# Performance work log

Measured on AMD Instinct MI355X. Metric: run time of the kernel, lower is better.

The kernel has to match this reference:

```python
import jax, jax.numpy as jnp
import numpy as np

N = 100000      # nodes
E = 1600000     # edges (avg degree 16)
IN, HID, OUT = 128, 32, 16
H = 2           # attention heads
EPS = 1e-5
NEG_SLOPE = 0.2


def setup_inputs() -> dict:
    key = jax.random.key(0)
    ks = jax.random.split(key, 24)
    f32 = jnp.float32
    def w(k, shape, scale=0.1):
        return jax.random.normal(k, shape, f32) * scale
    return {
        "x": jax.random.normal(ks[0], (N, IN), f32),
        "edge_index": jax.random.randint(ks[1], (2, E), 0, N, dtype=jnp.int32),
        # GCN layer 1
        "gcn1_W": w(ks[2], (IN, HID)), "gcn1_b": w(ks[3], (HID,)),
        # BN1 (eval mode: running stats)
        "bn1_g": 1.0 + w(ks[4], (HID,)), "bn1_b": w(ks[5], (HID,)),
        "bn1_m": w(ks[6], (HID,)), "bn1_v": 1.0 + jnp.abs(w(ks[7], (HID,))),
        # GAT layer 1 (HID -> HID, heads=H, concat=False)
        "gat1_W": w(ks[8], (HID, H * HID)), "gat1_as": w(ks[9], (H, HID)),
        "gat1_ad": w(ks[10], (H, HID)), "gat1_b": w(ks[11], (HID,)),
        # GCN layer 2
        "gcn2_W": w(ks[12], (HID, HID)), "gcn2_b": w(ks[13], (HID,)),
        # BN2
        "bn2_g": 1.0 + w(ks[14], (HID,)), "bn2_b": w(ks[15], (HID,)),
        "bn2_m": w(ks[16], (HID,)), "bn2_v": 1.0 + jnp.abs(w(ks[17], (HID,))),
        # GAT layer 2 (HID -> OUT, heads=H, concat=False)
        "gat2_W": w(ks[18], (HID, H * OUT)), "gat2_as": w(ks[19], (H, OUT)),
        "gat2_ad": w(ks[20], (H, OUT)), "gat2_b": w(ks[21], (OUT,)),
    }


def _add_self_loops(edge_index):
    loop = jnp.arange(N, dtype=edge_index.dtype)
    src = jnp.concatenate([edge_index[0], loop])
    dst = jnp.concatenate([edge_index[1], loop])
    return src, dst


def _gcn(x, src, dst, W, b):
    h = x @ W                                             # [N, F]
    deg = jax.ops.segment_sum(jnp.ones_like(dst, h.dtype), dst, N)
    dinv = jax.lax.rsqrt(jnp.maximum(deg, 1.0))
    norm = dinv[src] * dinv[dst]                          # [Etot]
    out = jax.ops.segment_sum(h[src] * norm[:, None], dst, N)
    return out + b


def _gat(x, src, dst, W, a_src, a_dst, b, F):
    # PyG GATConv (concat=False -> mean over heads); eval mode (no attn dropout)
    h = (x @ W).reshape(N, H, F)                          # [N, H, F]
    al_s = jnp.einsum('nhf,hf->nh', h, a_src)             # [N, H]
    al_d = jnp.einsum('nhf,hf->nh', h, a_dst)
    e = jax.nn.leaky_relu(al_s[src] + al_d[dst], NEG_SLOPE)  # [Etot, H]
    # segment softmax over destination neighborhoods (self-loops ensure >=1 edge)
    m = jax.ops.segment_max(e, dst, N)
    ex = jnp.exp(e - m[dst])
    s = jax.ops.segment_sum(ex, dst, N)
    alpha = ex / s[dst]                                   # [Etot, H]
    out = jax.ops.segment_sum(alpha[:, :, None] * h[src], dst, N)  # [N, H, F]
    return out.mean(axis=1) + b


def _bn_eval(x, g, b, m, v):
    return (x - m) * jax.lax.rsqrt(v + EPS) * g + b


def reference(x, edge_index, gcn1_W, gcn1_b, bn1_g, bn1_b, bn1_m, bn1_v,
              gat1_W, gat1_as, gat1_ad, gat1_b, gcn2_W, gcn2_b,
              bn2_g, bn2_b, bn2_m, bn2_v, gat2_W, gat2_as, gat2_ad, gat2_b):
    src, dst = _add_self_loops(edge_index)
    h = _gcn(x, src, dst, gcn1_W, gcn1_b)
    h = jax.nn.relu(_bn_eval(h, bn1_g, bn1_b, bn1_m, bn1_v))
    h = jax.nn.relu(_gat(h, src, dst, gat1_W, gat1_as, gat1_ad, gat1_b, HID))
    h = _gcn(h, src, dst, gcn2_W, gcn2_b)
    h = jax.nn.relu(_bn_eval(h, bn2_g, bn2_b, bn2_m, bn2_v))
    h = _gat(h, src, dst, gat2_W, gat2_as, gat2_ad, gat2_b, OUT)
    return jax.nn.log_softmax(h, axis=1)
```

## Files before the change

### kernel.cpp

```cpp
#include <hip/hip_runtime.h>
#include <hip/hip_bf16.h>

#define NN 100000
#define EE 1600000
#define SLAB 64
#define KB 391
#define CHUNK 4096

static constexpr float EPSV = 1e-5f;
static constexpr float SLOPE = 0.2f;

__device__ __forceinline__ float lrelu(float v) { return v > 0.f ? v : SLOPE * v; }

__device__ __forceinline__ unsigned rne_bf16(float v) {
    unsigned u = __float_as_uint(v);
    return (u + 0x7fffu + ((u >> 16) & 1u)) >> 16;
}
__device__ __forceinline__ float bf16_lo(unsigned u) { return __uint_as_float(u << 16); }
__device__ __forceinline__ float bf16_hi(unsigned u) { return __uint_as_float(u & 0xffff0000u); }


__global__ void k_z(int* __restrict__ hist) {
    int i = threadIdx.x;
    if (i < KB) hist[i] = 0;
}

__global__ __launch_bounds__(256) void k_hist(const int* __restrict__ dst, int* __restrict__ hist) {
    __shared__ int h[KB];
    int tid = threadIdx.x;
    for (int i = tid; i < KB; i += 256) h[i] = 0;
    __syncthreads();
    int e0 = blockIdx.x * CHUNK;
    #pragma unroll
    for (int r = 0; r < CHUNK / 256; ++r) {
        int e = e0 + r * 256 + tid;
        if (e < EE) atomicAdd(&h[dst[e] >> 8], 1);
    }
    __syncthreads();
    for (int i = tid; i < KB; i += 256)
        if (h[i]) atomicAdd(&hist[i], h[i]);
}

__global__ __launch_bounds__(512) void k_scan(const int* __restrict__ hist,
                                              int* __restrict__ start, int* __restrict__ gcur) {
    __shared__ int h[KB];
    int tid = threadIdx.x;
    for (int i = tid; i < KB; i += 512) h[i] = hist[i];
    __syncthreads();
    for (int t = tid; t < KB; t += 512) {
        int s = 0;
        for (int i = 0; i < t; ++i) s += h[i];
        start[t] = s;
        gcur[t] = 0;
    }
}

__global__ __launch_bounds__(256) void k_scat(const int* __restrict__ src, const int* __restrict__ dst,
                                              const int* __restrict__ start, int* __restrict__ gcur,
                                              unsigned int* __restrict__ ebuf) {
    __shared__ int hc[KB], hb[KB];
    int tid = threadIdx.x;
    for (int i = tid; i < KB; i += 256) hc[i] = 0;
    __syncthreads();
    int e0 = blockIdx.x * CHUNK;
    #pragma unroll
    for (int r = 0; r < CHUNK / 256; ++r) {
        int e = e0 + r * 256 + tid;
        if (e < EE) atomicAdd(&hc[dst[e] >> 8], 1);
    }
    __syncthreads();
    for (int i = tid; i < KB; i += 256) {
        int c = hc[i];
        if (c) hb[i] = atomicAdd(&gcur[i], c);
        hc[i] = 0;
    }
    __syncthreads();
    #pragma unroll
    for (int r = 0; r < CHUNK / 256; ++r) {
        int e = e0 + r * 256 + tid;
        if (e < EE) {
            int d = dst[e];
            int b = d >> 8;
            int rk = atomicAdd(&hc[b], 1);
            ebuf[start[b] + hb[b] + rk] = ((unsigned)src[e] << 8) | (unsigned)(d & 255);
        }
    }
}

__global__ __launch_bounds__(256) void k_bucket(const unsigned int* __restrict__ ebuf,
                                                const int* __restrict__ start, const int* __restrict__ hist,
                                                int* __restrict__ col, int* __restrict__ cnt) {
    __shared__ int lc[256];
    int tid = threadIdx.x;
    int b = blockIdx.x;
    lc[tid] = 0;
    __syncthreads();
    int s = start[b], nb = hist[b];
    for (int i = tid; i < nb; i += 256) {
        unsigned v = ebuf[s + i];
        int l = v & 255;
        int r = atomicAdd(&lc[l], 1);
        col[(((b << 8) + l) << 6) + r] = v >> 8;
    }
    __syncthreads();
    int node = (b << 8) + tid;
    if (node < NN) cnt[node] = lc[tid];
}

__global__ void k_deg(const int* __restrict__ cnt, float* __restrict__ dinv,
                      int* __restrict__ col) {
    int i = blockIdx.x * 256 + threadIdx.x;
    if (i < NN) {
        int c = cnt[i];
        dinv[i] = rsqrtf((float)(c + 1));
        col[i * SLAB + c] = i;
    }
}


__global__ __launch_bounds__(256) void k_gemm1(const float* __restrict__ x,
                                               const float* __restrict__ W,
                                               const float* __restrict__ dinv,
                                               unsigned* __restrict__ hsp) {
    __shared__ float xs[64][128];
    int tid = threadIdx.x;
    int lane = tid & 63;
    int wv = tid >> 6;
    int khalf = lane >> 5, f = lane & 31;
    float wreg[64];
    const float* wp = W + (khalf * 64) * 32 + f;
    #pragma unroll
    for (int i = 0; i < 64; ++i) wreg[i] = wp[i * 32];
    int n0 = blockIdx.x * 64;
    for (int i = tid; i < 64 * 32; i += 256) {
        int row = i >> 5, c4 = i & 31;
        int n = n0 + row;
        float4 v = (n < NN) ? *(const float4*)&x[(size_t)n * 128 + c4 * 4]
                            : make_float4(0.f, 0.f, 0.f, 0.f);
        *(float4*)&xs[row][c4 * 4] = v;
    }
    __syncthreads();
    #pragma unroll 4
    for (int t = 0; t < 16; ++t) {
        int row = wv * 16 + t;
        int n = n0 + row;
        if (n >= NN) break;
        const float* xp = &xs[row][khalf * 64];
        float a0 = 0.f, a1 = 0.f, a2 = 0.f, a3 = 0.f;
        #pragma unroll
        for (int j = 0; j < 16; j += 4) {
            float4 v0 = *(const float4*)&xp[(j + 0) * 4];
            float4 v1 = *(const float4*)&xp[(j + 1) * 4];
            float4 v2 = *(const float4*)&xp[(j + 2) * 4];
            float4 v3 = *(const float4*)&xp[(j + 3) * 4];
            a0 += v0.x * wreg[j * 4 + 0]  + v0.y * wreg[j * 4 + 1]  + v0.z * wreg[j * 4 + 2]  + v0.w * wreg[j * 4 + 3];
            a1 += v1.x * wreg[j * 4 + 4]  + v1.y * wreg[j * 4 + 5]  + v1.z * wreg[j * 4 + 6]  + v1.w * wreg[j * 4 + 7];
            a2 += v2.x * wreg[j * 4 + 8]  + v2.y * wreg[j * 4 + 9]  + v2.z * wreg[j * 4 + 10] + v2.w * wreg[j * 4 + 11];
            a3 += v3.x * wreg[j * 4 + 12] + v3.y * wreg[j * 4 + 13] + v3.z * wreg[j * 4 + 14] + v3.w * wreg[j * 4 + 15];
        }
        float tot = (a0 + a1) + (a2 + a3);
        tot += __shfl_xor(tot, 32);
        unsigned r16 = rne_bf16(tot * dinv[n]);
        unsigned hi16 = __shfl(r16, f + 1, 32);
        if (khalf == 0 && !(f & 1))
            hsp[n * 16 + (f >> 1)] = (hi16 << 16) | (r16 & 0xffffu);
    }
}


__global__ __launch_bounds__(256) void k_gcn1_gat1t(
    const unsigned* __restrict__ hsp, const int* __restrict__ cnt,
    const int* __restrict__ col, const float* __restrict__ dinv,
    const float* __restrict__ gb, const float* __restrict__ bng,
    const float* __restrict__ bnb, const float* __restrict__ bnm,
    const float* __restrict__ bnv,
    const float* __restrict__ W1, const float* __restrict__ as_, const float* __restrict__ ad_,
    unsigned* __restrict__ gp, float* __restrict__ al) {
    __shared__ float wAs[32][32], wBs[32][32];
    int tid = threadIdx.x;
    for (int i = tid; i < 1024; i += 256) {
        int k = i >> 5, f = i & 31;
        wAs[k][f] = W1[k * 64 + f];
        wBs[k][f] = W1[k * 64 + 32 + f];
    }
    __syncthreads();
    int r = tid >> 5, lane = tid & 31;
    int half = lane >> 4, l16 = lane & 15;
    int n = blockIdx.x * 8 + r;
    int dn = cnt[n] + 1;
    int base = n * SLAB;
    int c0 = col[base + lane];
    int c1 = (dn > 32) ? col[base + 32 + lane] : 0;
    float aL0 = 0.f, aH0 = 0.f, aL1 = 0.f, aH1 = 0.f;
    for (int j2 = 0; j2 < dn; j2 += 4) {
        int eA = j2 + half, eB = j2 + 2 + half;
        int cA = __shfl((j2 < 32) ? c0 : c1, eA & 31, 32);
        int cB = __shfl((j2 + 2 < 32) ? c0 : c1, eB & 31, 32);
        bool okA = eA < dn, okB = eB < dn;
        cA = okA ? cA : 0; cB = okB ? cB : 0;
        unsigned uA = hsp[cA * 16 + l16];
        unsigned uB = hsp[cB * 16 + l16];
        uA = okA ? uA : 0u; uB = okB ? uB : 0u;
        aL0 += bf16_lo(uA); aH0 += bf16_hi(uA);
        aL1 += bf16_lo(uB); aH1 += bf16_hi(uB);
    }
    float accLo = aL0 + aL1, accHi = aH0 + aH1;
    accLo += __shfl_xor(accLo, 16);
    accHi += __shfl_xor(accHi, 16);
    float vLo = __shfl(accLo, lane >> 1, 32);
    float vHi = __shfl(accHi, lane >> 1, 32);
    float acc = (lane & 1) ? vHi : vLo;
    float v = dinv[n] * acc + gb[lane];
    v = (v - bnm[lane]) * rsqrtf(bnv[lane] + EPSV) * bng[lane] + bnb[lane];
    v = fmaxf(v, 0.f);
    float gA0 = 0.f, gA1 = 0.f, gB0 = 0.f, gB1 = 0.f;
    #pragma unroll
    for (int k = 0; k < 32; k += 2) {
        float t0 = __shfl(v, k, 32);
        float t1v = __shfl(v, k + 1, 32);
        gA0 += t0 * wAs[k][lane];     gB0 += t0 * wBs[k][lane];
        gA1 += t1v * wAs[k + 1][lane]; gB1 += t1v * wBs[k + 1][lane];
    }
    float gA = gA0 + gA1, gB = gB0 + gB1;
    float pas0 = gA * as_[lane],      pad0 = gA * ad_[lane];
    float pas1 = gB * as_[32 + lane], pad1 = gB * ad_[32 + lane];
    #pragma unroll
    for (int off = 16; off; off >>= 1) {
        pas0 += __shfl_xor(pas0, off);
        pad0 += __shfl_xor(pad0, off);
        pas1 += __shfl_xor(pas1, off);
        pad1 += __shfl_xor(pad1, off);
    }
    if (lane == 0) *(float4*)&al[n * 4] = make_float4(pas0, pas1, pad0, pad1);
    gp[n * 32 + lane] = (rne_bf16(gB) << 16) | rne_bf16(gA);
}


__global__ __launch_bounds__(256) void k_gat1_pv(
    const unsigned* __restrict__ gp, const float* __restrict__ al,
    const int* __restrict__ cnt, const int* __restrict__ col,
    const float* __restrict__ b, const float* __restrict__ W2,
    const float* __restrict__ dinv, unsigned* __restrict__ hs3p) {
    __shared__ float2 ec[8][SLAB];
    __shared__ float w2s[32][32];
    int tid = threadIdx.x;
    for (int i = tid; i < 1024; i += 256) w2s[i >> 5][i & 31] = W2[i];
    __syncthreads();
    int r = tid >> 5, lane = tid & 31;
    int half = lane >> 4, l16 = lane & 15;
    int n = blockIdx.x * 8 + r;
    int dn = cnt[n] + 1;
    int base = n * SLAB;
    int c0 = col[base + lane];
    int c1 = (dn > 32) ? col[base + 32 + lane] : 0;
    float ad0 = al[n * 4 + 2], ad1 = al[n * 4 + 3];
    float e0a = -1e30f, e1a = -1e30f, e0b = -1e30f, e1b = -1e30f;
    if (lane < dn) {
        float4 a4 = *(const float4*)&al[(size_t)c0 * 4];
        e0a = lrelu(a4.x + ad0); e1a = lrelu(a4.y + ad1);
    }
    if (32 + lane < dn) {
        float4 a4 = *(const float4*)&al[(size_t)c1 * 4];
        e0b = lrelu(a4.x + ad0); e1b = lrelu(a4.y + ad1);
    }
    float m0 = fmaxf(e0a, e0b), m1 = fmaxf(e1a, e1b);
    #pragma unroll
    for (int off = 16; off; off >>= 1) {
        m0 = fmaxf(m0, __shfl_xor(m0, off));
        m1 = fmaxf(m1, __shfl_xor(m1, off));
    }
    float x0a = (lane < dn) ? __expf(e0a - m0) : 0.f;
    float x1a = (lane < dn) ? __expf(e1a - m1) : 0.f;
    float x0b = (32 + lane < dn) ? __expf(e0b - m0) : 0.f;
    float x1b = (32 + lane < dn) ? __expf(e1b - m1) : 0.f;
    ec[r][lane] = make_float2(x0a, x1a);
    ec[r][32 + lane] = make_float2(x0b, x1b);
    float s0 = x0a + x0b, s1 = x1a + x1b;
    #pragma unroll
    for (int off = 16; off; off >>= 1) {
        s0 += __shfl_xor(s0, off);
        s1 += __shfl_xor(s1, off);
    }
    const uint2* gp2 = (const uint2*)gp;
    float a0L = 0.f, a0H = 0.f, a1L = 0.f, a1H = 0.f;
    float b0L = 0.f, b0H = 0.f, b1L = 0.f, b1H = 0.f;
    for (int j2 = 0; j2 < dn; j2 += 4) {
        int eA = j2 + half, eB = j2 + 2 + half;
        int cA = __shfl((j2 < 32) ? c0 : c1, eA & 31, 32);
        int cB = __shfl((j2 + 2 < 32) ? c0 : c1, eB & 31, 32);
        bool okA = eA < dn, okB = eB < dn;
        cA = okA ? cA : 0; cB = okB ? cB : 0;
        uint2 uA = gp2[cA * 16 + l16];
        uint2 uB = gp2[cB * 16 + l16];
        float2 wA = ec[r][eA & 63];
        float2 wB = ec[r][eB & 63];
        uA.x = okA ? uA.x : 0u; uA.y = okA ? uA.y : 0u;
        uB.x = okB ? uB.x : 0u; uB.y = okB ? uB.y : 0u;
        a0L += wA.x * bf16_lo(uA.x); a1L += wA.y * bf16_hi(uA.x);
        a0H += wA.x * bf16_lo(uA.y); a1H += wA.y * bf16_hi(uA.y);
        b0L += wB.x * bf16_lo(uB.x); b1L += wB.y * bf16_hi(uB.x);
        b0H += wB.x * bf16_lo(uB.y); b1H += wB.y * bf16_hi(uB.y);
    }
    a0L += b0L; a0H += b0H; a1L += b1L; a1H += b1H;
    a0L += __shfl_xor(a0L, 16); a0H += __shfl_xor(a0H, 16);
    a1L += __shfl_xor(a1L, 16); a1H += __shfl_xor(a1H, 16);
    int p = lane >> 1;
    float t0L = __shfl(a0L, p, 32), t0H = __shfl(a0H, p, 32);
    float t1L = __shfl(a1L, p, 32), t1H = __shfl(a1H, p, 32);
    float A0 = (lane & 1) ? t0H : t0L;
    float A1 = (lane & 1) ? t1H : t1L;
    float v = 0.5f * (A0 / s0 + A1 / s1) + b[lane];
    v = fmaxf(v, 0.f);
    float g0 = 0.f, g1 = 0.f;
    #pragma unroll
    for (int k = 0; k < 32; k += 2) {
        g0 += __shfl(v, k, 32) * w2s[k][lane];
        g1 += __shfl(v, k + 1, 32) * w2s[k + 1][lane];
    }
    unsigned r16 = rne_bf16((g0 + g1) * dinv[n]);
    unsigned hi16 = __shfl(r16, lane + 1, 32);
    if (!(lane & 1)) hs3p[n * 16 + (lane >> 1)] = (hi16 << 16) | (r16 & 0xffffu);
}


__global__ __launch_bounds__(256) void k_gcn2_gat2t(
    const unsigned* __restrict__ hsp, const int* __restrict__ cnt,
    const int* __restrict__ col, const float* __restrict__ dinv,
    const float* __restrict__ gb, const float* __restrict__ bng,
    const float* __restrict__ bnb, const float* __restrict__ bnm,
    const float* __restrict__ bnv,
    const float* __restrict__ Wg, const float* __restrict__ as_, const float* __restrict__ ad_,
    unsigned* __restrict__ g2p, float* __restrict__ al) {
    __shared__ float wgs[32][32];
    int tid = threadIdx.x;
    for (int i = tid; i < 1024; i += 256) wgs[i >> 5][i & 31] = Wg[i];
    __syncthreads();
    int r = tid >> 5, lane = tid & 31;
    int half = lane >> 4, l16 = lane & 15;
    int n = blockIdx.x * 8 + r;
    int dn = cnt[n] + 1;
    int base = n * SLAB;
    int c0 = col[base + lane];
    int c1 = (dn > 32) ? col[base + 32 + lane] : 0;
    float aL0 = 0.f, aH0 = 0.f, aL1 = 0.f, aH1 = 0.f;
    for (int j2 = 0; j2 < dn; j2 += 4) {
        int eA = j2 + half, eB = j2 + 2 + half;
        int cA = __shfl((j2 < 32) ? c0 : c1, eA & 31, 32);
        int cB = __shfl((j2 + 2 < 32) ? c0 : c1, eB & 31, 32);
        bool okA = eA < dn, okB = eB < dn;
        cA = okA ? cA : 0; cB = okB ? cB : 0;
        unsigned uA = hsp[cA * 16 + l16];
        unsigned uB = hsp[cB * 16 + l16];
        uA = okA ? uA : 0u; uB = okB ? uB : 0u;
        aL0 += bf16_lo(uA); aH0 += bf16_hi(uA);
        aL1 += bf16_lo(uB); aH1 += bf16_hi(uB);
    }
    float accLo = aL0 + aL1, accHi = aH0 + aH1;
    accLo += __shfl_xor(accLo, 16);
    accHi += __shfl_xor(accHi, 16);
    float vLo = __shfl(accLo, lane >> 1, 32);
    float vHi = __shfl(accHi, lane >> 1, 32);
    float acc = (lane & 1) ? vHi : vLo;
    float v = dinv[n] * acc + gb[lane];
    v = (v - bnm[lane]) * rsqrtf(bnv[lane] + EPSV) * bng[lane] + bnb[lane];
    v = fmaxf(v, 0.f);
    float g0 = 0.f, g1 = 0.f;
    #pragma unroll
    for (int k = 0; k < 32; k += 2) {
        g0 += __shfl(v, k, 32) * wgs[k][lane];
        g1 += __shfl(v, k + 1, 32) * wgs[k + 1][lane];
    }
    float g = g0 + g1;
    int hh = lane >> 4, ff = lane & 15;
    float as_v = g * as_[hh * 16 + ff];
    float ad_v = g * ad_[hh * 16 + ff];
    #pragma unroll
    for (int off = 8; off; off >>= 1) {
        as_v += __shfl_xor(as_v, off);
        ad_v += __shfl_xor(ad_v, off);
    }
    if (ff == 0) { al[n * 4 + hh] = as_v; al[n * 4 + 2 + hh] = ad_v; }
    unsigned r16 = rne_bf16(g);
    unsigned hi16 = __shfl(r16, lane + 1, 32);
    if (!(lane & 1)) g2p[n * 16 + (lane >> 1)] = (hi16 << 16) | (r16 & 0xffffu);
}


__global__ __launch_bounds__(256) void k_gat2_agg(
    const unsigned* __restrict__ g2p, const float* __restrict__ al,
    const int* __restrict__ cnt, const int* __restrict__ col,
    const float* __restrict__ b, float* __restrict__ out) {
    __shared__ float2 ec[8][SLAB];
    int tid = threadIdx.x;
    int r = tid >> 5, lane = tid & 31;
    int half = lane >> 4, l16 = lane & 15;
    int n = blockIdx.x * 8 + r;
    int dn = cnt[n] + 1;
    int base = n * SLAB;
    int c0 = col[base + lane];
    int c1 = (dn > 32) ? col[base + 32 + lane] : 0;
    float ad0 = al[n * 4 + 2], ad1 = al[n * 4 + 3];
    float e0a = -1e30f, e1a = -1e30f, e0b = -1e30f, e1b = -1e30f;
    if (lane < dn) {
        float4 a4 = *(const float4*)&al[(size_t)c0 * 4];
        e0a = lrelu(a4.x + ad0); e1a = lrelu(a4.y + ad1);
    }
    if (32 + lane < dn) {
        float4 a4 = *(const float4*)&al[(size_t)c1 * 4];
        e0b = lrelu(a4.x + ad0); e1b = lrelu(a4.y + ad1);
    }
    float m0 = fmaxf(e0a, e0b), m1 = fmaxf(e1a, e1b);
    #pragma unroll
    for (int off = 16; off; off >>= 1) {
        m0 = fmaxf(m0, __shfl_xor(m0, off));
        m1 = fmaxf(m1, __shfl_xor(m1, off));
    }
    float x0a = (lane < dn) ? __expf(e0a - m0) : 0.f;
    float x1a = (lane < dn) ? __expf(e1a - m1) : 0.f;
    float x0b = (32 + lane < dn) ? __expf(e0b - m0) : 0.f;
    float x1b = (32 + lane < dn) ? __expf(e1b - m1) : 0.f;
    ec[r][lane] = make_float2(x0a, x1a);
    ec[r][32 + lane] = make_float2(x0b, x1b);
    float s0 = x0a + x0b, s1 = x1a + x1b;
    #pragma unroll
    for (int off = 16; off; off >>= 1) {
        s0 += __shfl_xor(s0, off);
        s1 += __shfl_xor(s1, off);
    }
    bool head1 = (l16 & 8) != 0;
    float aL0 = 0.f, aH0 = 0.f, aL1 = 0.f, aH1 = 0.f;
    for (int j2 = 0; j2 < dn; j2 += 4) {
        int eA = j2 + half, eB = j2 + 2 + half;
        int cA = __shfl((j2 < 32) ? c0 : c1, eA & 31, 32);
        int cB = __shfl((j2 + 2 < 32) ? c0 : c1, eB & 31, 32);
        bool okA = eA < dn, okB = eB < dn;
        cA = okA ? cA : 0; cB = okB ? cB : 0;
        unsigned uA = g2p[cA * 16 + l16];
        unsigned uB = g2p[cB * 16 + l16];
        float2 wA = ec[r][eA & 63];
        float2 wB = ec[r][eB & 63];
        float wa = head1 ? wA.y : wA.x;
        float wb = head1 ? wB.y : wB.x;
        uA = okA ? uA : 0u; uB = okB ? uB : 0u;
        aL0 += wa * bf16_lo(uA); aH0 += wa * bf16_hi(uA);
        aL1 += wb * bf16_lo(uB); aH1 += wb * bf16_hi(uB);
    }
    float accLo = aL0 + aL1, accHi = aH0 + aH1;
    accLo += __shfl_xor(accLo, 16);
    accHi += __shfl_xor(accHi, 16);
    float vLo = __shfl(accLo, lane >> 1, 32);
    float vHi = __shfl(accHi, lane >> 1, 32);
    float acc = (lane & 1) ? vHi : vLo;
    int hh = lane >> 4, ff = lane & 15;
    acc /= (hh ? s1 : s0);
    float v = 0.5f * (acc + __shfl_xor(acc, 16)) + b[ff];
    float mx = v;
    #pragma unroll
    for (int off = 8; off; off >>= 1) mx = fmaxf(mx, __shfl_xor(mx, off));
    float se = __expf(v - mx);
    #pragma unroll
    for (int off = 8; off; off >>= 1) se += __shfl_xor(se, off);
    if (hh == 0) out[(size_t)n * 16 + ff] = v - mx - __logf(se);
}


static inline size_t al256(size_t x) { return (x + 255) & ~((size_t)255); }

extern "C" void kernel_launch(void* const* d_in, const int* in_sizes, int n_in,
                              void* d_out, int out_size, void* d_ws, size_t ws_size,
                              hipStream_t stream) {
    const float* x      = (const float*)d_in[0];
    const int*   ei     = (const int*)d_in[1];
    const float* gcn1_W = (const float*)d_in[2];
    const float* gcn1_b = (const float*)d_in[3];
    const float* bn1_g  = (const float*)d_in[4];
    const float* bn1_b  = (const float*)d_in[5];
    const float* bn1_m  = (const float*)d_in[6];
    const float* bn1_v  = (const float*)d_in[7];
    const float* gat1_W = (const float*)d_in[8];
    const float* gat1_as= (const float*)d_in[9];
    const float* gat1_ad= (const float*)d_in[10];
    const float* gat1_b = (const float*)d_in[11];
    const float* gcn2_W = (const float*)d_in[12];
    const float* gcn2_b = (const float*)d_in[13];
    const float* bn2_g  = (const float*)d_in[14];
    const float* bn2_b  = (const float*)d_in[15];
    const float* bn2_m  = (const float*)d_in[16];
    const float* bn2_v  = (const float*)d_in[17];
    const float* gat2_W = (const float*)d_in[18];
    const float* gat2_as= (const float*)d_in[19];
    const float* gat2_ad= (const float*)d_in[20];
    const float* gat2_b = (const float*)d_in[21];
    float* out = (float*)d_out;

    char* w = (char*)d_ws;
    size_t off = 0;
    auto alloc = [&](size_t bytes) { void* p = w + off; off = al256(off + bytes); return p; };
    int*      cnt   = (int*)alloc((size_t)NN * 4);
    float*    dinv  = (float*)alloc((size_t)NN * 4);
    int*      col   = (int*)alloc((size_t)NN * SLAB * 4);
    unsigned* hsp   = (unsigned*)alloc((size_t)NN * 16 * 4);
    unsigned* g1p   = (unsigned*)alloc((size_t)NN * 32 * 4);
    unsigned* g2p   = (unsigned*)alloc((size_t)NN * 16 * 4);
    float*    al    = (float*)alloc((size_t)NN * 4 * 4);
    int*      hist  = (int*)alloc((size_t)KB * 4);
    int*      start = (int*)alloc((size_t)KB * 4);
    int*      gcur  = (int*)alloc((size_t)KB * 4);
    unsigned int* ebuf = (unsigned int*)g1p;

    const int* esrc = ei;
    const int* edst = ei + EE;
    const int GE = (EE + CHUNK - 1) / CHUNK;

    k_z<<<1, 512, 0, stream>>>(hist);
    k_hist<<<GE, 256, 0, stream>>>(edst, hist);
    k_scan<<<1, 512, 0, stream>>>(hist, start, gcur);
    k_scat<<<GE, 256, 0, stream>>>(esrc, edst, start, gcur, ebuf);
    k_bucket<<<KB, 256, 0, stream>>>(ebuf, start, hist, col, cnt);
    k_deg<<<(NN + 255) / 256, 256, 0, stream>>>(cnt, dinv, col);

    k_gemm1<<<(NN + 63) / 64, 256, 0, stream>>>(x, gcn1_W, dinv, hsp);
    k_gcn1_gat1t<<<NN / 8, 256, 0, stream>>>(hsp, cnt, col, dinv, gcn1_b,
                                             bn1_g, bn1_b, bn1_m, bn1_v,
                                             gat1_W, gat1_as, gat1_ad, g1p, al);
    k_gat1_pv<<<NN / 8, 256, 0, stream>>>(g1p, al, cnt, col, gat1_b,
                                          gcn2_W, dinv, hsp);
    k_gcn2_gat2t<<<NN / 8, 256, 0, stream>>>(hsp, cnt, col, dinv, gcn2_b,
                                             bn2_g, bn2_b, bn2_m, bn2_v,
                                             gat2_W, gat2_as, gat2_ad, g2p, al);
    k_gat2_agg<<<NN / 8, 256, 0, stream>>>(g2p, al, cnt, col, gat2_b, out);
}
```

Before: 295.8 us.

## Drop histogram/scan with fixed bucket slabs and add padded low-degree gather path

The CSR build no longer runs separate histogram and prefix-scan kernels. Each destination bucket now gets a fixed-capacity region in the edge buffer, filled through a per-bucket atomic counter. For nodes with at most 32 neighbours, column lists are padded with a dummy node whose feature row is zeroed. The four aggregation kernels then use a fully unrolled 8-step gather with wider vector loads and no per-edge bounds checks. The trade-off is wasted loads on padding entries and a fixed per-bucket capacity of 4736 edges, which would overflow on a skewed degree distribution.

Result: faster. 280.8 us (-5.1%).

```diff
diff --git a/kernel.cpp b/kernel.cpp
--- a/kernel.cpp
+++ b/kernel.cpp
@@ -6,6 +6,7 @@
 #define SLAB 64
 #define KB 391
 #define CHUNK 4096
+#define BSLAB 4736
 
 static constexpr float EPSV = 1e-5f;
 static constexpr float SLOPE = 0.2f;
@@ -20,44 +21,17 @@
 __device__ __forceinline__ float bf16_hi(unsigned u) { return __uint_as_float(u & 0xffff0000u); }
 
 
-__global__ void k_z(int* __restrict__ hist) {
+__global__ void k_z(int* __restrict__ bcnt, unsigned* __restrict__ hsp,
+                    unsigned* __restrict__ g1p, unsigned* __restrict__ g2p) {
     int i = threadIdx.x;
-    if (i < KB) hist[i] = 0;
-}
-
-__global__ __launch_bounds__(256) void k_hist(const int* __restrict__ dst, int* __restrict__ hist) {
-    __shared__ int h[KB];
-    int tid = threadIdx.x;
-    for (int i = tid; i < KB; i += 256) h[i] = 0;
-    __syncthreads();
-    int e0 = blockIdx.x * CHUNK;
-    #pragma unroll
-    for (int r = 0; r < CHUNK / 256; ++r) {
-        int e = e0 + r * 256 + tid;
-        if (e < EE) atomicAdd(&h[dst[e] >> 8], 1);
-    }
-    __syncthreads();
-    for (int i = tid; i < KB; i += 256)
-        if (h[i]) atomicAdd(&hist[i], h[i]);
-}
-
-__global__ __launch_bounds__(512) void k_scan(const int* __restrict__ hist,
-                                              int* __restrict__ start, int* __restrict__ gcur) {
-    __shared__ int h[KB];
-    int tid = threadIdx.x;
-    for (int i = tid; i < KB; i += 512) h[i] = hist[i];
-    __syncthreads();
-    for (int t = tid; t < KB; t += 512) {
-        int s = 0;
-        for (int i = 0; i < t; ++i) s += h[i];
-        start[t] = s;
-        gcur[t] = 0;
-    }
+    if (i < KB) bcnt[i] = 0;
+    if (i < 16) hsp[(size_t)NN * 16 + i] = 0u;
+    if (i < 32) g1p[(size_t)NN * 32 + i] = 0u;
+    if (i < 16) g2p[(size_t)NN * 16 + i] = 0u;
 }
 
 __global__ __launch_bounds__(256) void k_scat(const int* __restrict__ src, const int* __restrict__ dst,
-                                              const int* __restrict__ start, int* __restrict__ gcur,
-                                              unsigned int* __restrict__ ebuf) {
+                                              int* __restrict__ bcnt, unsigned int* __restrict__ ebuf) {
     __shared__ int hc[KB], hb[KB];
     int tid = threadIdx.x;
     for (int i = tid; i < KB; i += 256) hc[i] = 0;
@@ -71,7 +45,7 @@
     __syncthreads();
     for (int i = tid; i < KB; i += 256) {
         int c = hc[i];
-        if (c) hb[i] = atomicAdd(&gcur[i], c);
+        if (c) hb[i] = atomicAdd(&bcnt[i], c);
         hc[i] = 0;
     }
     __syncthreads();
@@ -82,20 +56,21 @@
             int d = dst[e];
             int b = d >> 8;
             int rk = atomicAdd(&hc[b], 1);
-            ebuf[start[b] + hb[b] + rk] = ((unsigned)src[e] << 8) | (unsigned)(d & 255);
+            ebuf[(size_t)b * BSLAB + hb[b] + rk] = ((unsigned)src[e] << 8) | (unsigned)(d & 255);
         }
     }
 }
 
 __global__ __launch_bounds__(256) void k_bucket(const unsigned int* __restrict__ ebuf,
-                                                const int* __restrict__ start, const int* __restrict__ hist,
+                                                const int* __restrict__ bcnt,
                                                 int* __restrict__ col, int* __restrict__ cnt) {
     __shared__ int lc[256];
     int tid = threadIdx.x;
     int b = blockIdx.x;
     lc[tid] = 0;
     __syncthreads();
-    int s = start[b], nb = hist[b];
+    size_t s = (size_t)b * BSLAB;
+    int nb = bcnt[b];
     for (int i = tid; i < nb; i += 256) {
         unsigned v = ebuf[s + i];
         int l = v & 255;
@@ -114,6 +89,7 @@
         int c = cnt[i];
         dinv[i] = rsqrtf((float)(c + 1));
         col[i * SLAB + c] = i;
+        for (int j = c + 1; j < 32; ++j) col[i * SLAB + j] = NN;
     }
 }
 
@@ -167,6 +143,54 @@
     }
 }
 
+__device__ __forceinline__ float quad_sum_hsp(const unsigned* hsp, int c0, int lane) {
+    int q = lane & 7, sub = lane >> 3;
+    const uint2* h2 = (const uint2*)hsp;
+    float ac0 = 0.f, ac1 = 0.f, ac2 = 0.f, ac3 = 0.f;
+    #pragma unroll
+    for (int s = 0; s < 8; ++s) {
+        int c = __shfl(c0, 4 * s + sub, 32);
+        uint2 u = h2[(size_t)c * 8 + q];
+        ac0 += bf16_lo(u.x); ac1 += bf16_hi(u.x);
+        ac2 += bf16_lo(u.y); ac3 += bf16_hi(u.y);
+    }
+    ac0 += __shfl_xor(ac0, 8); ac0 += __shfl_xor(ac0, 16);
+    ac1 += __shfl_xor(ac1, 8); ac1 += __shfl_xor(ac1, 16);
+    ac2 += __shfl_xor(ac2, 8); ac2 += __shfl_xor(ac2, 16);
+    ac3 += __shfl_xor(ac3, 8); ac3 += __shfl_xor(ac3, 16);
+    int p = lane >> 2;
+    float v0 = __shfl(ac0, p, 32), v1 = __shfl(ac1, p, 32);
+    float v2 = __shfl(ac2, p, 32), v3 = __shfl(ac3, p, 32);
+    float s01 = (lane & 1) ? v1 : v0;
+    float s23 = (lane & 1) ? v3 : v2;
+    return (lane & 2) ? s23 : s01;
+}
+
+__device__ __forceinline__ float gen_sum_hsp(const unsigned* hsp, const int* col, int base,
+                                             int dn, int lane) {
+    int half = lane >> 4, l16 = lane & 15;
+    int c0 = col[base + lane];
+    int c1 = col[base + 32 + lane];
+    float aL0 = 0.f, aH0 = 0.f, aL1 = 0.f, aH1 = 0.f;
+    for (int j2 = 0; j2 < dn; j2 += 4) {
+        int eA = j2 + half, eB = j2 + 2 + half;
+        int cA = __shfl((j2 < 32) ? c0 : c1, eA & 31, 32);
+        int cB = __shfl((j2 + 2 < 32) ? c0 : c1, eB & 31, 32);
+        bool okA = eA < dn, okB = eB < dn;
+        unsigned uA = hsp[(okA ? cA : 0) * 16 + l16];
+        unsigned uB = hsp[(okB ? cB : 0) * 16 + l16];
+        uA = okA ? uA : 0u; uB = okB ? uB : 0u;
+        aL0 += bf16_lo(uA); aH0 += bf16_hi(uA);
+        aL1 += bf16_lo(uB); aH1 += bf16_hi(uB);
+    }
+    float accLo = aL0 + aL1, accHi = aH0 + aH1;
+    accLo += __shfl_xor(accLo, 16);
+    accHi += __shfl_xor(accHi, 16);
+    float vLo = __shfl(accLo, lane >> 1, 32);
+    float vHi = __shfl(accHi, lane >> 1, 32);
+    return (lane & 1) ? vHi : vLo;
+}
+
 
 __global__ __launch_bounds__(256) void k_gcn1_gat1t(
     const unsigned* __restrict__ hsp, const int* __restrict__ cnt,
@@ -185,31 +209,12 @@
     }
     __syncthreads();
     int r = tid >> 5, lane = tid & 31;
-    int half = lane >> 4, l16 = lane & 15;
     int n = blockIdx.x * 8 + r;
     int dn = cnt[n] + 1;
     int base = n * SLAB;
-    int c0 = col[base + lane];
-    int c1 = (dn > 32) ? col[base + 32 + lane] : 0;
-    float aL0 = 0.f, aH0 = 0.f, aL1 = 0.f, aH1 = 0.f;
-    for (int j2 = 0; j2 < dn; j2 += 4) {
-        int eA = j2 + half, eB = j2 + 2 + half;
-        int cA = __shfl((j2 < 32) ? c0 : c1, eA & 31, 32);
-        int cB = __shfl((j2 + 2 < 32) ? c0 : c1, eB & 31, 32);
-        bool okA = eA < dn, okB = eB < dn;
-        cA = okA ? cA : 0; cB = okB ? cB : 0;
-        unsigned uA = hsp[cA * 16 + l16];
-        unsigned uB = hsp[cB * 16 + l16];
-        uA = okA ? uA : 0u; uB = okB ? uB : 0u;
-        aL0 += bf16_lo(uA); aH0 += bf16_hi(uA);
-        aL1 += bf16_lo(uB); aH1 += bf16_hi(uB);
-    }
-    float accLo = aL0 + aL1, accHi = aH0 + aH1;
-    accLo += __shfl_xor(accLo, 16);
-    accHi += __shfl_xor(accHi, 16);
-    float vLo = __shfl(accLo, lane >> 1, 32);
-    float vHi = __shfl(accHi, lane >> 1, 32);
-    float acc = (lane & 1) ? vHi : vLo;
+    float acc;
+    if (dn <= 32) acc = quad_sum_hsp(hsp, col[base + lane], lane);
+    else          acc = gen_sum_hsp(hsp, col, base, dn, lane);
     float v = dinv[n] * acc + gb[lane];
     v = (v - bnm[lane]) * rsqrtf(bnv[lane] + EPSV) * bng[lane] + bnb[lane];
     v = fmaxf(v, 0.f);
@@ -247,12 +252,11 @@
     for (int i = tid; i < 1024; i += 256) w2s[i >> 5][i & 31] = W2[i];
     __syncthreads();
     int r = tid >> 5, lane = tid & 31;
-    int half = lane >> 4, l16 = lane & 15;
     int n = blockIdx.x * 8 + r;
     int dn = cnt[n] + 1;
     int base = n * SLAB;
     int c0 = col[base + lane];
-    int c1 = (dn > 32) ? col[base + 32 + lane] : 0;
+    int c1 = (dn > 32) ? col[base + 32 + lane] : (int)NN;
     float ad0 = al[n * 4 + 2], ad1 = al[n * 4 + 3];
     float e0a = -1e30f, e1a = -1e30f, e0b = -1e30f, e1b = -1e30f;
     if (lane < dn) {
@@ -281,34 +285,70 @@
         s0 += __shfl_xor(s0, off);
         s1 += __shfl_xor(s1, off);
     }
-    const uint2* gp2 = (const uint2*)gp;
-    float a0L = 0.f, a0H = 0.f, a1L = 0.f, a1H = 0.f;
-    float b0L = 0.f, b0H = 0.f, b1L = 0.f, b1H = 0.f;
-    for (int j2 = 0; j2 < dn; j2 += 4) {
-        int eA = j2 + half, eB = j2 + 2 + half;
-        int cA = __shfl((j2 < 32) ? c0 : c1, eA & 31, 32);
-        int cB = __shfl((j2 + 2 < 32) ? c0 : c1, eB & 31, 32);
-        bool okA = eA < dn, okB = eB < dn;
-        cA = okA ? cA : 0; cB = okB ? cB : 0;
-        uint2 uA = gp2[cA * 16 + l16];
-        uint2 uB = gp2[cB * 16 + l16];
-        float2 wA = ec[r][eA & 63];
-        float2 wB = ec[r][eB & 63];
-        uA.x = okA ? uA.x : 0u; uA.y = okA ? uA.y : 0u;
-        uB.x = okB ? uB.x : 0u; uB.y = okB ? uB.y : 0u;
-        a0L += wA.x * bf16_lo(uA.x); a1L += wA.y * bf16_hi(uA.x);
-        a0H += wA.x * bf16_lo(uA.y); a1H += wA.y * bf16_hi(uA.y);
-        b0L += wB.x * bf16_lo(uB.x); b1L += wB.y * bf16_hi(uB.x);
-        b0H += wB.x * bf16_lo(uB.y); b1H += wB.y * bf16_hi(uB.y);
-    }
-    a0L += b0L; a0H += b0H; a1L += b1L; a1H += b1H;
-    a0L += __shfl_xor(a0L, 16); a0H += __shfl_xor(a0H, 16);
-    a1L += __shfl_xor(a1L, 16); a1H += __shfl_xor(a1H, 16);
-    int p = lane >> 1;
-    float t0L = __shfl(a0L, p, 32), t0H = __shfl(a0H, p, 32);
-    float t1L = __shfl(a1L, p, 32), t1H = __shfl(a1H, p, 32);
-    float A0 = (lane & 1) ? t0H : t0L;
-    float A1 = (lane & 1) ? t1H : t1L;
+    float A0, A1;
+    if (dn <= 32) {
+        int q = lane & 7, sub = lane >> 3;
+        const uint4* g4 = (const uint4*)gp;
+        float aL0 = 0.f, aL1 = 0.f, aL2 = 0.f, aL3 = 0.f;
+        float aH0 = 0.f, aH1 = 0.f, aH2 = 0.f, aH3 = 0.f;
+        #pragma unroll
+        for (int s = 0; s < 8; ++s) {
+            int e = 4 * s + sub;
+            int c = __shfl(c0, e, 32);
+            uint4 u = g4[(size_t)c * 8 + q];
+            float2 wv = ec[r][e];
+            aL0 += wv.x * bf16_lo(u.x); aH0 += wv.y * bf16_hi(u.x);
+            aL1 += wv.x * bf16_lo(u.y); aH1 += wv.y * bf16_hi(u.y);
+            aL2 += wv.x * bf16_lo(u.z); aH2 += wv.y * bf16_hi(u.z);
+            aL3 += wv.x * bf16_lo(u.w); aH3 += wv.y * bf16_hi(u.w);
+        }
+        aL0 += __shfl_xor(aL0, 8); aL0 += __shfl_xor(aL0, 16);
+        aL1 += __shfl_xor(aL1, 8); aL1 += __shfl_xor(aL1, 16);
+        aL2 += __shfl_xor(aL2, 8); aL2 += __shfl_xor(aL2, 16);
+        aL3 += __shfl_xor(aL3, 8); aL3 += __shfl_xor(aL3, 16);
+        aH0 += __shfl_xor(aH0, 8); aH0 += __shfl_xor(aH0, 16);
+        aH1 += __shfl_xor(aH1, 8); aH1 += __shfl_xor(aH1, 16);
+        aH2 += __shfl_xor(aH2, 8); aH2 += __shfl_xor(aH2, 16);
+        aH3 += __shfl_xor(aH3, 8); aH3 += __shfl_xor(aH3, 16);
+        int p = lane >> 2;
+        float l0 = __shfl(aL0, p, 32), l1 = __shfl(aL1, p, 32);
+        float l2 = __shfl(aL2, p, 32), l3 = __shfl(aL3, p, 32);
+        float h0 = __shfl(aH0, p, 32), h1 = __shfl(aH1, p, 32);
+        float h2 = __shfl(aH2, p, 32), h3 = __shfl(aH3, p, 32);
+        float sl01 = (lane & 1) ? l1 : l0, sl23 = (lane & 1) ? l3 : l2;
+        float sh01 = (lane & 1) ? h1 : h0, sh23 = (lane & 1) ? h3 : h2;
+        A0 = (lane & 2) ? sl23 : sl01;
+        A1 = (lane & 2) ? sh23 : sh01;
+    } else {
+        int half = lane >> 4, l16 = lane & 15;
+        const uint2* gp2 = (const uint2*)gp;
+        float a0L = 0.f, a0H = 0.f, a1L = 0.f, a1H = 0.f;
+        float b0L = 0.f, b0H = 0.f, b1L = 0.f, b1H = 0.f;
+        for (int j2 = 0; j2 < dn; j2 += 4) {
+            int eA = j2 + half, eB = j2 + 2 + half;
+            int cA = __shfl((j2 < 32) ? c0 : c1, eA & 31, 32);
+            int cB = __shfl((j2 + 2 < 32) ? c0 : c1, eB & 31, 32);
+            bool okA = eA < dn, okB = eB < dn;
+            uint2 uA = gp2[(size_t)(okA ? cA : 0) * 16 + l16];
+            uint2 uB = gp2[(size_t)(okB ? cB : 0) * 16 + l16];
+            float2 wA = ec[r][eA & 63];
+            float2 wB = ec[r][eB & 63];
+            uA.x = okA ? uA.x : 0u; uA.y = okA ? uA.y : 0u;
+            uB.x = okB ? uB.x : 0u; uB.y = okB ? uB.y : 0u;
+            a0L += wA.x * bf16_lo(uA.x); a1L += wA.y * bf16_hi(uA.x);
+            a0H += wA.x * bf16_lo(uA.y); a1H += wA.y * bf16_hi(uA.y);
+            b0L += wB.x * bf16_lo(uB.x); b1L += wB.y * bf16_hi(uB.x);
+            b0H += wB.x * bf16_lo(uB.y); b1H += wB.y * bf16_hi(uB.y);
+        }
+        a0L += b0L; a0H += b0H; a1L += b1L; a1H += b1H;
+        a0L += __shfl_xor(a0L, 16); a0H += __shfl_xor(a0H, 16);
+        a1L += __shfl_xor(a1L, 16); a1H += __shfl_xor(a1H, 16);
+        int p = lane >> 1;
+        float t0L = __shfl(a0L, p, 32), t0H = __shfl(a0H, p, 32);
+        float t1L = __shfl(a1L, p, 32), t1H = __shfl(a1H, p, 32);
+        A0 = (lane & 1) ? t0H : t0L;
+        A1 = (lane & 1) ? t1H : t1L;
+    }
     float v = 0.5f * (A0 / s0 + A1 / s1) + b[lane];
     v = fmaxf(v, 0.f);
     float g0 = 0.f, g1 = 0.f;
@@ -336,31 +376,12 @@
     for (int i = tid; i < 1024; i += 256) wgs[i >> 5][i & 31] = Wg[i];
     __syncthreads();
     int r = tid >> 5, lane = tid & 31;
-    int half = lane >> 4, l16 = lane & 15;
     int n = blockIdx.x * 8 + r;
     int dn = cnt[n] + 1;
     int base = n * SLAB;
-    int c0 = col[base + lane];
-    int c1 = (dn > 32) ? col[base + 32 + lane] : 0;
-    float aL0 = 0.f, aH0 = 0.f, aL1 = 0.f, aH1 = 0.f;
-    for (int j2 = 0; j2 < dn; j2 += 4) {
-        int eA = j2 + half, eB = j2 + 2 + half;
-        int cA = __shfl((j2 < 32) ? c0 : c1, eA & 31, 32);
-        int cB = __shfl((j2 + 2 < 32) ? c0 : c1, eB & 31, 32);
-        bool okA = eA < dn, okB = eB < dn;
-        cA = okA ? cA : 0; cB = okB ? cB : 0;
-        unsigned uA = hsp[cA * 16 + l16];
-        unsigned uB = hsp[cB * 16 + l16];
-        uA = okA ? uA : 0u; uB = okB ? uB : 0u;
-        aL0 += bf16_lo(uA); aH0 += bf16_hi(uA);
-        aL1 += bf16_lo(uB); aH1 += bf16_hi(uB);
-    }
-    float accLo = aL0 + aL1, accHi = aH0 + aH1;
-    accLo += __shfl_xor(accLo, 16);
-    accHi += __shfl_xor(accHi, 16);
-    float vLo = __shfl(accLo, lane >> 1, 32);
-    float vHi = __shfl(accHi, lane >> 1, 32);
-    float acc = (lane & 1) ? vHi : vLo;
+    float acc;
+    if (dn <= 32) acc = quad_sum_hsp(hsp, col[base + lane], lane);
+    else          acc = gen_sum_hsp(hsp, col, base, dn, lane);
     float v = dinv[n] * acc + gb[lane];
     v = (v - bnm[lane]) * rsqrtf(bnv[lane] + EPSV) * bng[lane] + bnb[lane];
     v = fmaxf(v, 0.f);
@@ -393,12 +414,11 @@
     __shared__ float2 ec[8][SLAB];
     int tid = threadIdx.x;
     int r = tid >> 5, lane = tid & 31;
-    int half = lane >> 4, l16 = lane & 15;
     int n = blockIdx.x * 8 + r;
     int dn = cnt[n] + 1;
     int base = n * SLAB;
     int c0 = col[base + lane];
-    int c1 = (dn > 32) ? col[base + 32 + lane] : 0;
+    int c1 = (dn > 32) ? col[base + 32 + lane] : (int)NN;
     float ad0 = al[n * 4 + 2], ad1 = al[n * 4 + 3];
     float e0a = -1e30f, e1a = -1e30f, e0b = -1e30f, e1b = -1e30f;
     if (lane < dn) {
@@ -427,30 +447,58 @@
         s0 += __shfl_xor(s0, off);
         s1 += __shfl_xor(s1, off);
     }
-    bool head1 = (l16 & 8) != 0;
-    float aL0 = 0.f, aH0 = 0.f, aL1 = 0.f, aH1 = 0.f;
-    for (int j2 = 0; j2 < dn; j2 += 4) {
-        int eA = j2 + half, eB = j2 + 2 + half;
-        int cA = __shfl((j2 < 32) ? c0 : c1, eA & 31, 32);
-        int cB = __shfl((j2 + 2 < 32) ? c0 : c1, eB & 31, 32);
-        bool okA = eA < dn, okB = eB < dn;
-        cA = okA ? cA : 0; cB = okB ? cB : 0;
-        unsigned uA = g2p[cA * 16 + l16];
-        unsigned uB = g2p[cB * 16 + l16];
-        float2 wA = ec[r][eA & 63];
-        float2 wB = ec[r][eB & 63];
-        float wa = head1 ? wA.y : wA.x;
-        float wb = head1 ? wB.y : wB.x;
-        uA = okA ? uA : 0u; uB = okB ? uB : 0u;
-        aL0 += wa * bf16_lo(uA); aH0 += wa * bf16_hi(uA);
-        aL1 += wb * bf16_lo(uB); aH1 += wb * bf16_hi(uB);
-    }
-    float accLo = aL0 + aL1, accHi = aH0 + aH1;
-    accLo += __shfl_xor(accLo, 16);
-    accHi += __shfl_xor(accHi, 16);
-    float vLo = __shfl(accLo, lane >> 1, 32);
-    float vHi = __shfl(accHi, lane >> 1, 32);
-    float acc = (lane & 1) ? vHi : vLo;
+    float acc;
+    if (dn <= 32) {
+        int q = lane & 7, sub = lane >> 3;
+        bool head1 = (lane & 4) != 0;
+        const uint2* g2 = (const uint2*)g2p;
+        float ac0 = 0.f, ac1 = 0.f, ac2 = 0.f, ac3 = 0.f;
+        #pragma unroll
+        for (int s = 0; s < 8; ++s) {
+            int e = 4 * s + sub;
+            int c = __shfl(c0, e, 32);
+            uint2 u = g2[(size_t)c * 8 + q];
+            float2 wv = ec[r][e];
+            float w = head1 ? wv.y : wv.x;
+            ac0 += w * bf16_lo(u.x); ac1 += w * bf16_hi(u.x);
+            ac2 += w * bf16_lo(u.y); ac3 += w * bf16_hi(u.y);
+        }
+        ac0 += __shfl_xor(ac0, 8); ac0 += __shfl_xor(ac0, 16);
+        ac1 += __shfl_xor(ac1, 8); ac1 += __shfl_xor(ac1, 16);
+        ac2 += __shfl_xor(ac2, 8); ac2 += __shfl_xor(ac2, 16);
+        ac3 += __shfl_xor(ac3, 8); ac3 += __shfl_xor(ac3, 16);
+        int p = lane >> 2;
+        float v0 = __shfl(ac0, p, 32), v1 = __shfl(ac1, p, 32);
+        float v2 = __shfl(ac2, p, 32), v3 = __shfl(ac3, p, 32);
+        float s01 = (lane & 1) ? v1 : v0;
+        float s23 = (lane & 1) ? v3 : v2;
+        acc = (lane & 2) ? s23 : s01;
+    } else {
+        int half = lane >> 4, l16 = lane & 15;
+        bool head1g = (l16 & 8) != 0;
+        float aL0 = 0.f, aH0 = 0.f, aL1 = 0.f, aH1 = 0.f;
+        for (int j2 = 0; j2 < dn; j2 += 4) {
+            int eA = j2 + half, eB = j2 + 2 + half;
+            int cA = __shfl((j2 < 32) ? c0 : c1, eA & 31, 32);
+            int cB = __shfl((j2 + 2 < 32) ? c0 : c1, eB & 31, 32);
+            bool okA = eA < dn, okB = eB < dn;
+            unsigned uA = g2p[(okA ? cA : 0) * 16 + l16];
+            unsigned uB = g2p[(okB ? cB : 0) * 16 + l16];
+            float2 wA = ec[r][eA & 63];
+            float2 wB = ec[r][eB & 63];
+            float wa = head1g ? wA.y : wA.x;
+            float wb = head1g ? wB.y : wB.x;
+            uA = okA ? uA : 0u; uB = okB ? uB : 0u;
+            aL0 += wa * bf16_lo(uA); aH0 += wa * bf16_hi(uA);
+            aL1 += wb * bf16_lo(uB); aH1 += wb * bf16_hi(uB);
+        }
+        float accLo = aL0 + aL1, accHi = aH0 + aH1;
+        accLo += __shfl_xor(accLo, 16);
+        accHi += __shfl_xor(accHi, 16);
+        float vLo = __shfl(accLo, lane >> 1, 32);
+        float vHi = __shfl(accHi, lane >> 1, 32);
+        acc = (lane & 1) ? vHi : vLo;
+    }
     int hh = lane >> 4, ff = lane & 15;
     acc /= (hh ? s1 : s0);
     float v = 0.5f * (acc + __shfl_xor(acc, 16)) + b[ff];
@@ -499,24 +547,20 @@
     int*      cnt   = (int*)alloc((size_t)NN * 4);
     float*    dinv  = (float*)alloc((size_t)NN * 4);
     int*      col   = (int*)alloc((size_t)NN * SLAB * 4);
-    unsigned* hsp   = (unsigned*)alloc((size_t)NN * 16 * 4);
-    unsigned* g1p   = (unsigned*)alloc((size_t)NN * 32 * 4);
-    unsigned* g2p   = (unsigned*)alloc((size_t)NN * 16 * 4);
+    unsigned* hsp   = (unsigned*)alloc((size_t)(NN + 1) * 16 * 4);
+    unsigned* g1p   = (unsigned*)alloc((size_t)(NN + 1) * 32 * 4);
+    unsigned* g2p   = (unsigned*)alloc((size_t)(NN + 1) * 16 * 4);
     float*    al    = (float*)alloc((size_t)NN * 4 * 4);
-    int*      hist  = (int*)alloc((size_t)KB * 4);
-    int*      start = (int*)alloc((size_t)KB * 4);
-    int*      gcur  = (int*)alloc((size_t)KB * 4);
+    int*      bcnt  = (int*)alloc((size_t)KB * 4);
     unsigned int* ebuf = (unsigned int*)g1p;
 
     const int* esrc = ei;
     const int* edst = ei + EE;
     const int GE = (EE + CHUNK - 1) / CHUNK;
 
-    k_z<<<1, 512, 0, stream>>>(hist);
-    k_hist<<<GE, 256, 0, stream>>>(edst, hist);
-    k_scan<<<1, 512, 0, stream>>>(hist, start, gcur);
-    k_scat<<<GE, 256, 0, stream>>>(esrc, edst, start, gcur, ebuf);
-    k_bucket<<<KB, 256, 0, stream>>>(ebuf, start, hist, col, cnt);
+    k_z<<<1, 512, 0, stream>>>(bcnt, hsp, g1p, g2p);
+    k_scat<<<GE, 256, 0, stream>>>(esrc, edst, bcnt, ebuf);
+    k_bucket<<<KB, 256, 0, stream>>>(ebuf, bcnt, col, cnt);
     k_deg<<<(NN + 255) / 256, 256, 0, stream>>>(cnt, dinv, col);
 
     k_gemm1<<<(NN + 63) / 64, 256, 0, stream>>>(x, gcn1_W, dinv, hsp);
```
